# Kernel optimization log

Hardware: AMD Instinct MI355X
Metric: run time of the kernel (lower is better)

Reference implementation:

```python
import jax, jax.numpy as jnp
import numpy as np

B, IN_CH, N, DIM, PH, HID, K = 4, 128, 2048, 256, 64, 1024, 16
EPS = 1e-5


def conv1(x, w, b):
    # 1x1 Conv1d: x (B,C,N), w (O,C) -> (B,O,N)
    return jnp.einsum('oc,bcn->bon', w, x) + b[None, :, None]


def conv2(x, w, b):
    # 1x1 Conv2d: x (B,C,N,K), w (O,C) -> (B,O,N,K)
    return jnp.einsum('oc,bcnk->bonk', w, x) + b[None, :, None, None]


def bn2(x, g, beta, mean, var):
    # eval-mode BatchNorm2d over channel dim of (B,C,N,K)
    scale = g * jax.lax.rsqrt(var + EPS)
    return x * scale[None, :, None, None] + (beta - mean * scale)[None, :, None, None]


def query_knn(pos, k):
    # pos: (B,3,N). Returns (B,N,K) indices of k nearest neighbors (incl. self).
    p = jnp.transpose(pos, (0, 2, 1))                     # (B,N,3)
    sq = jnp.sum(p * p, axis=-1)                          # (B,N)
    dist = sq[:, :, None] + sq[:, None, :] - 2.0 * jnp.einsum('bnc,bmc->bnm', p, p)
    _, idx = jax.lax.top_k(-dist, k)                      # smallest distances first
    return idx


def group(feat, idx):
    # feat: (B,C,N), idx: (B,N,K) -> (B,C,N,K) where out[b,c,i,k]=feat[b,c,idx[b,i,k]]
    b, c, n = feat.shape
    k = idx.shape[-1]
    ib = jnp.broadcast_to(idx.reshape(b, 1, n * k), (b, c, n * k))
    return jnp.take_along_axis(feat, ib, axis=2).reshape(b, c, n, k)


def setup_inputs() -> dict:
    key = jax.random.key(0)
    ks = jax.random.split(key, 12)
    s = 0.02
    return {
        'x': jax.random.normal(ks[0], (B, IN_CH, N), jnp.float32),
        'pos': jax.random.normal(ks[1], (B, 3, N), jnp.float32),
        'ls_w': jax.random.normal(ks[2], (DIM, IN_CH), jnp.float32) * s,
        'ls_b': jnp.zeros((DIM,), jnp.float32),
        'kw': jax.random.normal(ks[3], (DIM, DIM), jnp.float32) * s,
        'kb': jnp.zeros((DIM,), jnp.float32),
        'qw': jax.random.normal(ks[4], (DIM, DIM), jnp.float32) * s,
        'qb': jnp.zeros((DIM,), jnp.float32),
        'vw': jax.random.normal(ks[5], (DIM, DIM), jnp.float32) * s,
        'vb': jnp.zeros((DIM,), jnp.float32),
        'pw1': jax.random.normal(ks[6], (PH, 3), jnp.float32) * s,
        'pb1': jnp.zeros((PH,), jnp.float32),
        'pg': jnp.ones((PH,), jnp.float32),
        'pbeta': jnp.zeros((PH,), jnp.float32),
        'pmean': jnp.zeros((PH,), jnp.float32),
        'pvar': jnp.ones((PH,), jnp.float32),
        'pw2': jax.random.normal(ks[7], (DIM, PH), jnp.float32) * s,
        'pb2': jnp.zeros((DIM,), jnp.float32),
        'aw1': jax.random.normal(ks[8], (HID, DIM), jnp.float32) * s,
        'ab1': jnp.zeros((HID,), jnp.float32),
        'ag': jnp.ones((HID,), jnp.float32),
        'abeta': jnp.zeros((HID,), jnp.float32),
        'amean': jnp.zeros((HID,), jnp.float32),
        'avar': jnp.ones((HID,), jnp.float32),
        'aw2': jax.random.normal(ks[9], (DIM, HID), jnp.float32) * s,
        'ab2': jnp.zeros((DIM,), jnp.float32),
        'lw': jax.random.normal(ks[10], (IN_CH, DIM), jnp.float32) * s,
        'lb': jnp.zeros((IN_CH,), jnp.float32),
    }


def reference(x, pos, ls_w, ls_b, kw, kb, qw, qb, vw, vb,
              pw1, pb1, pg, pbeta, pmean, pvar, pw2, pb2,
              aw1, ab1, ag, abeta, amean, avar, aw2, ab2, lw, lb):
    identity = x
    h = conv1(x, ls_w, ls_b)                              # (B,DIM,N)
    idx = query_knn(pos, K)                               # (B,N,K) int32
    key_f = group(conv1(h, kw, kb), idx)                  # (B,DIM,N,K)
    value = conv1(h, vw, vb)                              # (B,DIM,N)
    query = conv1(h, qw, qb)                              # (B,DIM,N)
    qk_rel = query[:, :, :, None] - key_f                 # (B,DIM,N,K)
    pos_rel = pos[:, :, :, None] - group(pos, idx)        # (B,3,N,K)
    pe = conv2(jax.nn.relu(bn2(conv2(pos_rel, pw1, pb1), pg, pbeta, pmean, pvar)), pw2, pb2)
    attn = conv2(jax.nn.relu(bn2(conv2(qk_rel + pe, aw1, ab1), ag, abeta, amean, avar)), aw2, ab2)
    attn = jax.nn.softmax(attn, axis=-1)                  # softmax over K
    val_g = group(value, idx) + pe                        # (B,DIM,N,K)
    agg = jnp.sum(attn * val_g, axis=-1)                  # (B,DIM,N)
    y = conv1(agg, lw, lb)                                # (B,IN_CH,N)
    return y + identity
```

## Files before the change

### kernel.cpp

```cpp
#include <hip/hip_runtime.h>
#include <hip/hip_bf16.h>
#include <math.h>

#define B_    4
#define CIN   128
#define NPTS  2048
#define DIM   256
#define PH    64
#define HIDN  1024
#define KNN_  16
#define BN    (B_*NPTS)
#define CC    (BN*KNN_)
#define EPS_  1e-5f

typedef __bf16 bf16;
typedef __bf16 bf16x8 __attribute__((ext_vector_type(8)));
typedef __bf16 bf16x4 __attribute__((ext_vector_type(4)));
typedef float  f32x4  __attribute__((ext_vector_type(4)));

__global__ __launch_bounds__(256) void prep_kernel(
    const float* __restrict__ ls_w, const float* __restrict__ kw,
    const float* __restrict__ qw,   const float* __restrict__ vw,
    const float* __restrict__ pw2,  const float* __restrict__ aw1,
    const float* __restrict__ aw2,  const float* __restrict__ lw,
    const float* __restrict__ pb1,  const float* __restrict__ pg,
    const float* __restrict__ pbeta,const float* __restrict__ pmean,
    const float* __restrict__ pvar,
    const float* __restrict__ ab1,  const float* __restrict__ ag,
    const float* __restrict__ abeta,const float* __restrict__ amean,
    const float* __restrict__ avar,
    bf16* ls_wb, bf16* kwb, bf16* qwb, bf16* vwb,
    bf16* pw2b, bf16* aw1b, bf16* aw2b, bf16* lwb,
    float* pe_scale, float* pe_shift, float* at_scale, float* at_shift)
{
  long e = (long)blockIdx.x * 256 + threadIdx.x;
  if (e < 32768)  { ls_wb[e] = (bf16)ls_w[e]; return; } e -= 32768;
  if (e < 65536)  { kwb[e]   = (bf16)kw[e];   return; } e -= 65536;
  if (e < 65536)  { qwb[e]   = (bf16)qw[e];   return; } e -= 65536;
  if (e < 65536)  { vwb[e]   = (bf16)vw[e];   return; } e -= 65536;
  if (e < 16384)  { pw2b[e]  = (bf16)pw2[e];  return; } e -= 16384;
  if (e < 262144) { aw1b[e]  = (bf16)aw1[e];  return; } e -= 262144;
  if (e < 262144) { aw2b[e]  = (bf16)aw2[e];  return; } e -= 262144;
  if (e < 32768)  { lwb[e]   = (bf16)lw[e];   return; } e -= 32768;
  if (e < 64) {
    float sc = pg[e] * rsqrtf(pvar[e] + EPS_);
    pe_scale[e] = sc;
    pe_shift[e] = sc * pb1[e] + pbeta[e] - pmean[e] * sc;
    return;
  } e -= 64;
  if (e < 1024) {
    float sc = ag[e] * rsqrtf(avar[e] + EPS_);
    at_scale[e] = sc;
    at_shift[e] = sc * ab1[e] + abeta[e] - amean[e] * sc;
  }
}

__global__ __launch_bounds__(256) void transpose_x_kernel(
    const float* __restrict__ x, bf16* __restrict__ xT)
{
  long e = (long)blockIdx.x * 256 + threadIdx.x;
  int ch = (int)(e & (CIN - 1));
  long i = e >> 7;
  int n = (int)(i & (NPTS - 1));
  int b = (int)(i >> 11);
  xT[e] = (bf16)x[((long)b * CIN + ch) * NPTS + n];
}

__global__ __launch_bounds__(256) void knn_kernel(
    const float* __restrict__ pos, int* __restrict__ idx_out)
{
  __shared__ float px[NPTS], py[NPTS], pz[NPTS];
  const int tid = threadIdx.x;
  const int lane = tid & 63, wave = tid >> 6;
  const int q = blockIdx.x * 4 + wave;
  const int b = q >> 11;
  const int n = q & (NPTS - 1);
  const float* p = pos + (long)b * 3 * NPTS;
  for (int j = tid; j < NPTS; j += 256) {
    px[j] = p[j]; py[j] = p[NPTS + j]; pz[j] = p[2 * NPTS + j];
  }
  __syncthreads();
  float qx = px[n], qy = py[n], qz = pz[n];
  float qs = qx * qx + qy * qy + qz * qz;
  float d[32];
#pragma unroll
  for (int j = 0; j < 32; ++j) {
    int pt = j * 64 + lane;
    float x = px[pt], y = py[pt], z = pz[pt];
    float s2 = x * x + y * y + z * z;
    float dt = qx * x + qy * y + qz * z;
    d[j] = qs + s2 - 2.f * dt;
  }
  for (int r = 0; r < KNN_; ++r) {
    float bv = 1e30f; int bj = 0;
#pragma unroll
    for (int j = 0; j < 32; ++j)
      if (d[j] < bv) { bv = d[j]; bj = j; }
    int bi = bj * 64 + lane;
#pragma unroll
    for (int off = 32; off >= 1; off >>= 1) {
      float ov = __shfl_xor(bv, off);
      int   oi = __shfl_xor(bi, off);
      if (ov < bv || (ov == bv && oi < bi)) { bv = ov; bi = oi; }
    }
    if (lane == 0) idx_out[(long)q * KNN_ + r] = bi;
#pragma unroll
    for (int j = 0; j < 32; ++j)
      if (bi == j * 64 + lane) d[j] = 1e30f;
  }
}

template<int KD, bool OBF16>
__global__ __launch_bounds__(256) void gemmT_kernel(
    const bf16* __restrict__ inT, const bf16* __restrict__ Wb,
    const float* __restrict__ bias, void* __restrict__ outp, int O)
{
  const int tid = threadIdx.x;
  const int lane = tid & 63, wave = tid >> 6;
  const int row16 = lane & 15, grp = lane >> 4;
  const long i0 = (long)blockIdx.x * 64 + (wave & 1) * 32;
  const long o0 = (long)blockIdx.y * 64 + (wave >> 1) * 32;
  f32x4 acc[2][2] = {};
  const bf16* a0p = inT + (i0 + row16) * KD + grp * 8;
  const bf16* a1p = a0p + 16 * KD;
  const bf16* b0p = Wb + (o0 + row16) * KD + grp * 8;
  const bf16* b1p = b0p + 16 * KD;
#pragma unroll
  for (int ks = 0; ks < KD / 32; ++ks) {
    bf16x8 a0 = *(const bf16x8*)(a0p + ks * 32);
    bf16x8 a1 = *(const bf16x8*)(a1p + ks * 32);
    bf16x8 b0 = *(const bf16x8*)(b0p + ks * 32);
    bf16x8 b1 = *(const bf16x8*)(b1p + ks * 32);
    acc[0][0] = __builtin_amdgcn_mfma_f32_16x16x32_bf16(a0, b0, acc[0][0], 0, 0, 0);
    acc[0][1] = __builtin_amdgcn_mfma_f32_16x16x32_bf16(a0, b1, acc[0][1], 0, 0, 0);
    acc[1][0] = __builtin_amdgcn_mfma_f32_16x16x32_bf16(a1, b0, acc[1][0], 0, 0, 0);
    acc[1][1] = __builtin_amdgcn_mfma_f32_16x16x32_bf16(a1, b1, acc[1][1], 0, 0, 0);
  }
#pragma unroll
  for (int ot = 0; ot < 2; ++ot) {
    long o = o0 + ot * 16 + row16;
    float bv = bias[o];
#pragma unroll
    for (int it = 0; it < 2; ++it) {
#pragma unroll
      for (int r = 0; r < 4; ++r) {
        long i = i0 + it * 16 + grp * 4 + r;
        float v = acc[it][ot][r] + bv;
        if (OBF16) ((bf16*)outp)[i * O + o] = (bf16)v;
        else       ((float*)outp)[i * O + o] = v;
      }
    }
  }
}

__global__ __launch_bounds__(256, 2) void attn_fused_kernel(
    const bf16* __restrict__ qT, const bf16* __restrict__ kT,
    const bf16* __restrict__ vTb, const float* __restrict__ pos,
    const int* __restrict__ idx, const float* __restrict__ pw1,
    const float* __restrict__ pe_scale, const float* __restrict__ pe_shift,
    const bf16* __restrict__ pw2b, const float* __restrict__ pb2,
    const bf16* __restrict__ aw1b, const bf16* __restrict__ aw2b,
    const float* __restrict__ at_scale, const float* __restrict__ at_shift,
    const float* __restrict__ ab2, bf16* __restrict__ aggT)
{
  __shared__ __align__(16) bf16 u_lds[64][264];
  __shared__ __align__(16) bf16 tbuf[64 * 136];
  __shared__ float rel_lds[64][4];
  __shared__ int   idx_lds[64];
  bf16 (*t_lds)[136]  = (bf16(*)[136])tbuf;
  bf16 (*hid_lds)[72] = (bf16(*)[72])tbuf;

  const int tid = threadIdx.x;
  const int lane = tid & 63, wave = tid >> 6;
  const int row16 = lane & 15, grp = lane >> 4;
  const long c0 = (long)blockIdx.x * 64;
  const int bn0 = blockIdx.x * 4;
  const int b = bn0 >> 11;
  const float* pB = pos + (long)b * 3 * NPTS;
  const int os = wave * 64;

  if (tid < 64) {
    int nb = idx[c0 + tid];
    idx_lds[tid] = nb;
    int n = (bn0 + (tid >> 4)) & (NPTS - 1);
    rel_lds[tid][0] = pB[n] - pB[nb];
    rel_lds[tid][1] = pB[NPTS + n] - pB[NPTS + nb];
    rel_lds[tid][2] = pB[2 * NPTS + n] - pB[2 * NPTS + nb];
  }
#pragma unroll
  for (int it = 0; it < 8; ++it) {
    int id = it * 256 + tid;
    int col = id >> 5, ch16 = id & 31;
    int nb = idx[c0 + col];
    *(bf16x8*)&u_lds[col][ch16 * 8] =
        *(const bf16x8*)(kT + ((long)b * NPTS + nb) * DIM + ch16 * 8);
  }
  __syncthreads();

  {
    int c = tid & 63, jq = tid >> 6;
    float rx = rel_lds[c][0], ry = rel_lds[c][1], rz = rel_lds[c][2];
#pragma unroll
    for (int jj = 0; jj < 16; ++jj) {
      int j = jq * 16 + jj;
      float v = pw1[j * 3] * rx + pw1[j * 3 + 1] * ry + pw1[j * 3 + 2] * rz;
      v = pe_scale[j] * v + pe_shift[j];
      hid_lds[c][j] = (bf16)fmaxf(v, 0.f);
    }
  }
  __syncthreads();

  f32x4 accpe[4][4] = {};
#pragma unroll
  for (int ks = 0; ks < 2; ++ks) {
    bf16x8 ah[4];
#pragma unroll
    for (int ct = 0; ct < 4; ++ct)
      ah[ct] = *(const bf16x8*)&hid_lds[ct * 16 + row16][ks * 32 + grp * 8];
#pragma unroll
    for (int ot = 0; ot < 4; ++ot) {
      bf16x8 bw = *(const bf16x8*)(pw2b + (long)(os + ot * 16 + row16) * PH + ks * 32 + grp * 8);
#pragma unroll
      for (int ct = 0; ct < 4; ++ct)
        accpe[ct][ot] = __builtin_amdgcn_mfma_f32_16x16x32_bf16(ah[ct], bw, accpe[ct][ot], 0, 0, 0);
    }
  }

  bf16x4 pe_bf[4][4];
#pragma unroll
  for (int ot = 0; ot < 4; ++ot) {
    int o = os + ot * 16 + row16;
    float pb2v = pb2[o];
#pragma unroll
    for (int ct = 0; ct < 4; ++ct) {
      float qv = (float)qT[(long)(bn0 + ct) * DIM + o];
#pragma unroll
      for (int r = 0; r < 4; ++r) {
        int c = ct * 16 + grp * 4 + r;
        float pev = accpe[ct][ot][r] + pb2v;
        float kv = (float)u_lds[c][o];
        u_lds[c][o] = (bf16)(qv - kv + pev);
        pe_bf[ct][ot][r] = (bf16)pev;
      }
    }
  }
  __syncthreads();

  const int hs = wave * 32;
  f32x4 acc2[4][4] = {};
  for (int jc = 0; jc < 8; ++jc) {
    const int hg = jc * 128 + hs;
    f32x4 acc1[4][2] = {};
#pragma unroll
    for (int ks = 0; ks < 8; ++ks) {
      bf16x8 bu[4], aw[2];
#pragma unroll
      for (int ct = 0; ct < 4; ++ct)
        bu[ct] = *(const bf16x8*)&u_lds[ct * 16 + row16][ks * 32 + grp * 8];
#pragma unroll
      for (int jt = 0; jt < 2; ++jt)
        aw[jt] = *(const bf16x8*)(aw1b + (long)(hg + jt * 16 + row16) * DIM + ks * 32 + grp * 8);
#pragma unroll
      for (int ct = 0; ct < 4; ++ct)
#pragma unroll
        for (int jt = 0; jt < 2; ++jt)
          acc1[ct][jt] = __builtin_amdgcn_mfma_f32_16x16x32_bf16(aw[jt], bu[ct], acc1[ct][jt], 0, 0, 0);
    }
#pragma unroll
    for (int jt = 0; jt < 2; ++jt) {
      f32x4 sc4 = *(const f32x4*)&at_scale[hg + jt * 16 + grp * 4];
      f32x4 sh4 = *(const f32x4*)&at_shift[hg + jt * 16 + grp * 4];
#pragma unroll
      for (int ct = 0; ct < 4; ++ct) {
        bf16x4 pk;
#pragma unroll
        for (int r = 0; r < 4; ++r) {
          float v = sc4[r] * acc1[ct][jt][r] + sh4[r];
          pk[r] = (bf16)fmaxf(v, 0.f);
        }
        *(bf16x4*)&t_lds[ct * 16 + row16][hs + jt * 16 + grp * 4] = pk;
      }
    }
    __syncthreads();
#pragma unroll
    for (int ks2 = 0; ks2 < 4; ++ks2) {
      bf16x8 a2[4], b2;
#pragma unroll
      for (int ct = 0; ct < 4; ++ct)
        a2[ct] = *(const bf16x8*)&t_lds[ct * 16 + row16][ks2 * 32 + grp * 8];
#pragma unroll
      for (int ot = 0; ot < 4; ++ot) {
        b2 = *(const bf16x8*)(aw2b + (long)(os + ot * 16 + row16) * HIDN + jc * 128 + ks2 * 32 + grp * 8);
#pragma unroll
        for (int ct = 0; ct < 4; ++ct)
          acc2[ct][ot] = __builtin_amdgcn_mfma_f32_16x16x32_bf16(a2[ct], b2, acc2[ct][ot], 0, 0, 0);
      }
    }
    __syncthreads();
  }

#pragma unroll
  for (int ct = 0; ct < 4; ++ct) {
#pragma unroll
    for (int ot = 0; ot < 4; ++ot) {
      int o = os + ot * 16 + row16;
      float ab = ab2[o];
      float l[4];
      float m = -1e30f;
#pragma unroll
      for (int r = 0; r < 4; ++r) {
        l[r] = acc2[ct][ot][r] + ab;
        m = fmaxf(m, l[r]);
      }
      m = fmaxf(m, __shfl_xor(m, 16));
      m = fmaxf(m, __shfl_xor(m, 32));
      float s = 0.f;
#pragma unroll
      for (int r = 0; r < 4; ++r) { l[r] = expf(l[r] - m); s += l[r]; }
      s += __shfl_xor(s, 16);
      s += __shfl_xor(s, 32);
      float inv = 1.f / s;
      float agg = 0.f;
#pragma unroll
      for (int r = 0; r < 4; ++r) {
        int c = ct * 16 + grp * 4 + r;
        int nb = idx_lds[c];
        float vv = (float)vTb[((long)b * NPTS + nb) * DIM + o];
        agg += l[r] * (vv + (float)pe_bf[ct][ot][r]);
      }
      agg *= inv;
      agg += __shfl_xor(agg, 16);
      agg += __shfl_xor(agg, 32);
      if (grp == 0) aggT[(long)(bn0 + ct) * DIM + o] = (bf16)agg;
    }
  }
}

__global__ __launch_bounds__(256) void final_kernel(
    const bf16* __restrict__ aggT, const bf16* __restrict__ lwb,
    const float* __restrict__ lb, const float* __restrict__ x,
    float* __restrict__ out)
{
  const int tid = threadIdx.x;
  const int lane = tid & 63, wave = tid >> 6;
  const int row16 = lane & 15, grp = lane >> 4;
  const long i0 = (long)blockIdx.x * 64 + (wave & 1) * 32;
  const int o0 = blockIdx.y * 64 + (wave >> 1) * 32;
  f32x4 acc[2][2] = {};
  const bf16* a0p = aggT + (i0 + row16) * DIM + grp * 8;
  const bf16* a1p = a0p + 16 * DIM;
  const bf16* b0p = lwb + (long)(o0 + row16) * DIM + grp * 8;
  const bf16* b1p = b0p + 16 * DIM;
#pragma unroll
  for (int ks = 0; ks < 8; ++ks) {
    bf16x8 a0 = *(const bf16x8*)(a0p + ks * 32);
    bf16x8 a1 = *(const bf16x8*)(a1p + ks * 32);
    bf16x8 b0 = *(const bf16x8*)(b0p + ks * 32);
    bf16x8 b1 = *(const bf16x8*)(b1p + ks * 32);
    acc[0][0] = __builtin_amdgcn_mfma_f32_16x16x32_bf16(a0, b0, acc[0][0], 0, 0, 0);
    acc[0][1] = __builtin_amdgcn_mfma_f32_16x16x32_bf16(a0, b1, acc[0][1], 0, 0, 0);
    acc[1][0] = __builtin_amdgcn_mfma_f32_16x16x32_bf16(a1, b0, acc[1][0], 0, 0, 0);
    acc[1][1] = __builtin_amdgcn_mfma_f32_16x16x32_bf16(a1, b1, acc[1][1], 0, 0, 0);
  }
#pragma unroll
  for (int ot = 0; ot < 2; ++ot) {
    int o = o0 + ot * 16 + row16;
    float bv = lb[o];
#pragma unroll
    for (int it = 0; it < 2; ++it) {
#pragma unroll
      for (int r = 0; r < 4; ++r) {
        long i = i0 + it * 16 + grp * 4 + r;
        int bb = (int)(i >> 11);
        int n = (int)(i & (NPTS - 1));
        long off = ((long)bb * CIN + o) * NPTS + n;
        out[off] = acc[it][ot][r] + bv + x[off];
      }
    }
  }
}

extern "C" void kernel_launch(void* const* d_in, const int* in_sizes, int n_in,
                              void* d_out, int out_size, void* d_ws, size_t ws_size,
                              hipStream_t stream)
{
  const float* x     = (const float*)d_in[0];
  const float* pos   = (const float*)d_in[1];
  const float* ls_w  = (const float*)d_in[2];
  const float* ls_b  = (const float*)d_in[3];
  const float* kw    = (const float*)d_in[4];
  const float* kb    = (const float*)d_in[5];
  const float* qw    = (const float*)d_in[6];
  const float* qb    = (const float*)d_in[7];
  const float* vw    = (const float*)d_in[8];
  const float* vb    = (const float*)d_in[9];
  const float* pw1   = (const float*)d_in[10];
  const float* pb1   = (const float*)d_in[11];
  const float* pg    = (const float*)d_in[12];
  const float* pbeta = (const float*)d_in[13];
  const float* pmean = (const float*)d_in[14];
  const float* pvar  = (const float*)d_in[15];
  const float* pw2   = (const float*)d_in[16];
  const float* pb2   = (const float*)d_in[17];
  const float* aw1   = (const float*)d_in[18];
  const float* ab1   = (const float*)d_in[19];
  const float* ag    = (const float*)d_in[20];
  const float* abeta = (const float*)d_in[21];
  const float* amean = (const float*)d_in[22];
  const float* avar  = (const float*)d_in[23];
  const float* aw2   = (const float*)d_in[24];
  const float* ab2   = (const float*)d_in[25];
  const float* lw    = (const float*)d_in[26];
  const float* lb    = (const float*)d_in[27];

  char* ws = (char*)d_ws;
  size_t off = 0;
  auto alloc = [&](size_t bytes) -> void* {
    void* p = ws + off;
    off = (off + bytes + 255) & ~(size_t)255;
    return p;
  };

  bf16* ls_wb = (bf16*)alloc(32768 * 2);
  bf16* kwb   = (bf16*)alloc(65536 * 2);
  bf16* qwb   = (bf16*)alloc(65536 * 2);
  bf16* vwb   = (bf16*)alloc(65536 * 2);
  bf16* pw2b  = (bf16*)alloc(16384 * 2);
  bf16* aw1b  = (bf16*)alloc(262144 * 2);
  bf16* aw2b  = (bf16*)alloc(262144 * 2);
  bf16* lwb   = (bf16*)alloc(32768 * 2);
  float* pe_scale = (float*)alloc(64 * 4);
  float* pe_shift = (float*)alloc(64 * 4);
  float* at_scale = (float*)alloc(1024 * 4);
  float* at_shift = (float*)alloc(1024 * 4);
  int*  idx  = (int*)alloc((size_t)CC * 4);
  bf16* xT   = (bf16*)alloc((size_t)BN * CIN * 2);
  bf16* hT   = (bf16*)alloc((size_t)BN * DIM * 2);
  bf16* qT   = (bf16*)alloc((size_t)BN * DIM * 2);
  bf16* kT   = (bf16*)alloc((size_t)BN * DIM * 2);
  bf16* vTb  = (bf16*)alloc((size_t)BN * DIM * 2);
  bf16* aggT = (bf16*)alloc((size_t)BN * DIM * 2);

  prep_kernel<<<dim3((803904 + 255) / 256), 256, 0, stream>>>(
      ls_w, kw, qw, vw, pw2, aw1, aw2, lw,
      pb1, pg, pbeta, pmean, pvar, ab1, ag, abeta, amean, avar,
      ls_wb, kwb, qwb, vwb, pw2b, aw1b, aw2b, lwb,
      pe_scale, pe_shift, at_scale, at_shift);

  transpose_x_kernel<<<dim3(BN * CIN / 256), 256, 0, stream>>>(x, xT);

  knn_kernel<<<dim3(BN / 4), 256, 0, stream>>>(pos, idx);

  gemmT_kernel<128, true><<<dim3(BN / 64, DIM / 64), 256, 0, stream>>>(xT, ls_wb, ls_b, hT, DIM);

  gemmT_kernel<256, true><<<dim3(BN / 64, DIM / 64), 256, 0, stream>>>(hT, qwb, qb, qT, DIM);
  gemmT_kernel<256, true><<<dim3(BN / 64, DIM / 64), 256, 0, stream>>>(hT, kwb, kb, kT, DIM);
  gemmT_kernel<256, true><<<dim3(BN / 64, DIM / 64), 256, 0, stream>>>(hT, vwb, vb, vTb, DIM);

  attn_fused_kernel<<<dim3(CC / 64), 256, 0, stream>>>(
      qT, kT, vTb, pos, idx, pw1, pe_scale, pe_shift, pw2b, pb2,
      aw1b, aw2b, at_scale, at_shift, ab2, aggT);

  final_kernel<<<dim3(BN / 64, CIN / 64), 256, 0, stream>>>(aggT, lwb, lb, x, (float*)d_out);
}
```

Baseline: 513.9 us.

## Precompose attention first layer with q/k/pos projections to shrink per-neighbor GEMM

Uses linearity of aw1 over (q - k + pe): precomputes aw1·Wq and aw1·Wk as weight products, computes per-point A1q and A1k (BN x 1024), and composes aw1·pw2 into a 1024x64 matrix. The per-neighbor first attention GEMM drops from K=256 to K=64 over the hidden features, plus gathered A1k rows. The trade is extra point-level GEMMs and larger gathered rows (1024 bf16 per neighbor) with different bf16 rounding. Occupancy hint raised to 4 blocks since the large u_lds buffer is removed.

```diff
diff --git a/kernel.cpp b/kernel.cpp
--- a/kernel.cpp
+++ b/kernel.cpp
@@ -19,29 +19,36 @@
 typedef float  f32x4  __attribute__((ext_vector_type(4)));
 
 __global__ __launch_bounds__(256) void prep_kernel(
-    const float* __restrict__ ls_w, const float* __restrict__ kw,
-    const float* __restrict__ qw,   const float* __restrict__ vw,
+    const float* __restrict__ ls_w, const float* __restrict__ qw,
+    const float* __restrict__ kw,   const float* __restrict__ vw,
     const float* __restrict__ pw2,  const float* __restrict__ aw1,
     const float* __restrict__ aw2,  const float* __restrict__ lw,
+    const float* __restrict__ qb,   const float* __restrict__ kb,
+    const float* __restrict__ pb2,
     const float* __restrict__ pb1,  const float* __restrict__ pg,
     const float* __restrict__ pbeta,const float* __restrict__ pmean,
     const float* __restrict__ pvar,
     const float* __restrict__ ab1,  const float* __restrict__ ag,
     const float* __restrict__ abeta,const float* __restrict__ amean,
     const float* __restrict__ avar,
-    bf16* ls_wb, bf16* kwb, bf16* qwb, bf16* vwb,
-    bf16* pw2b, bf16* aw1b, bf16* aw2b, bf16* lwb,
-    float* pe_scale, float* pe_shift, float* at_scale, float* at_shift)
+    bf16* ls_wb, bf16* vwb, bf16* qwt, bf16* kwt,
+    bf16* pw2b, bf16* pw2t, bf16* aw1b, bf16* aw2b, bf16* lwb,
+    float* pe_scale, float* pe_shift, float* at_scale, float* at_shift,
+    float* bq, float* bk, float* zeros)
 {
   long e = (long)blockIdx.x * 256 + threadIdx.x;
   if (e < 32768)  { ls_wb[e] = (bf16)ls_w[e]; return; } e -= 32768;
-  if (e < 65536)  { kwb[e]   = (bf16)kw[e];   return; } e -= 65536;
-  if (e < 65536)  { qwb[e]   = (bf16)qw[e];   return; } e -= 65536;
   if (e < 65536)  { vwb[e]   = (bf16)vw[e];   return; } e -= 65536;
-  if (e < 16384)  { pw2b[e]  = (bf16)pw2[e];  return; } e -= 16384;
-  if (e < 262144) { aw1b[e]  = (bf16)aw1[e];  return; } e -= 262144;
-  if (e < 262144) { aw2b[e]  = (bf16)aw2[e];  return; } e -= 262144;
-  if (e < 32768)  { lwb[e]   = (bf16)lw[e];   return; } e -= 32768;
+  if (e < 65536)  { int c = (int)(e >> 8), o = (int)(e & 255);
+                    qwt[e] = (bf16)qw[o * 256 + c]; return; } e -= 65536;
+  if (e < 65536)  { int c = (int)(e >> 8), o = (int)(e & 255);
+                    kwt[e] = (bf16)kw[o * 256 + c]; return; } e -= 65536;
+  if (e < 16384)  { pw2b[e] = (bf16)pw2[e];   return; } e -= 16384;
+  if (e < 16384)  { int ph = (int)(e >> 8), o = (int)(e & 255);
+                    pw2t[e] = (bf16)pw2[o * 64 + ph]; return; } e -= 16384;
+  if (e < 262144) { aw1b[e] = (bf16)aw1[e];   return; } e -= 262144;
+  if (e < 262144) { aw2b[e] = (bf16)aw2[e];   return; } e -= 262144;
+  if (e < 32768)  { lwb[e]  = (bf16)lw[e];    return; } e -= 32768;
   if (e < 64) {
     float sc = pg[e] * rsqrtf(pvar[e] + EPS_);
     pe_scale[e] = sc;
@@ -52,7 +59,19 @@
     float sc = ag[e] * rsqrtf(avar[e] + EPS_);
     at_scale[e] = sc;
     at_shift[e] = sc * ab1[e] + abeta[e] - amean[e] * sc;
-  }
+    return;
+  } e -= 1024;
+  if (e < 1024) {
+    float s = 0.f;
+    for (int o = 0; o < 256; ++o) s += aw1[e * 256 + o] * (qb[o] + pb2[o]);
+    bq[e] = s; return;
+  } e -= 1024;
+  if (e < 1024) {
+    float s = 0.f;
+    for (int o = 0; o < 256; ++o) s += aw1[e * 256 + o] * kb[o];
+    bk[e] = s; return;
+  } e -= 1024;
+  if (e < 1024) { zeros[e] = 0.f; }
 }
 
 __global__ __launch_bounds__(256) void transpose_x_kernel(
@@ -153,22 +172,20 @@
   }
 }
 
-__global__ __launch_bounds__(256, 2) void attn_fused_kernel(
-    const bf16* __restrict__ qT, const bf16* __restrict__ kT,
+__global__ __launch_bounds__(256, 4) void attn_fused_kernel(
     const bf16* __restrict__ vTb, const float* __restrict__ pos,
     const int* __restrict__ idx, const float* __restrict__ pw1,
     const float* __restrict__ pe_scale, const float* __restrict__ pe_shift,
     const bf16* __restrict__ pw2b, const float* __restrict__ pb2,
-    const bf16* __restrict__ aw1b, const bf16* __restrict__ aw2b,
+    const bf16* __restrict__ Mwb, const bf16* __restrict__ A1q,
+    const bf16* __restrict__ A1k, const bf16* __restrict__ aw2b,
     const float* __restrict__ at_scale, const float* __restrict__ at_shift,
     const float* __restrict__ ab2, bf16* __restrict__ aggT)
 {
-  __shared__ __align__(16) bf16 u_lds[64][264];
-  __shared__ __align__(16) bf16 tbuf[64 * 136];
+  __shared__ __align__(16) bf16 hid_lds[64][72];
+  __shared__ __align__(16) bf16 t_lds[64][136];
   __shared__ float rel_lds[64][4];
   __shared__ int   idx_lds[64];
-  bf16 (*t_lds)[136]  = (bf16(*)[136])tbuf;
-  bf16 (*hid_lds)[72] = (bf16(*)[72])tbuf;
 
   const int tid = threadIdx.x;
   const int lane = tid & 63, wave = tid >> 6;
@@ -178,6 +195,7 @@
   const int b = bn0 >> 11;
   const float* pB = pos + (long)b * 3 * NPTS;
   const int os = wave * 64;
+  const int hs = wave * 32;
 
   if (tid < 64) {
     int nb = idx[c0 + tid];
@@ -187,14 +205,6 @@
     rel_lds[tid][1] = pB[NPTS + n] - pB[NPTS + nb];
     rel_lds[tid][2] = pB[2 * NPTS + n] - pB[2 * NPTS + nb];
   }
-#pragma unroll
-  for (int it = 0; it < 8; ++it) {
-    int id = it * 256 + tid;
-    int col = id >> 5, ch16 = id & 31;
-    int nb = idx[c0 + col];
-    *(bf16x8*)&u_lds[col][ch16 * 8] =
-        *(const bf16x8*)(kT + ((long)b * NPTS + nb) * DIM + ch16 * 8);
-  }
   __syncthreads();
 
   {
@@ -210,6 +220,10 @@
   }
   __syncthreads();
 
+  int nbv[4];
+#pragma unroll
+  for (int ct = 0; ct < 4; ++ct) nbv[ct] = idx_lds[ct * 16 + row16];
+
   f32x4 accpe[4][4] = {};
 #pragma unroll
   for (int ks = 0; ks < 2; ++ks) {
@@ -225,57 +239,49 @@
         accpe[ct][ot] = __builtin_amdgcn_mfma_f32_16x16x32_bf16(ah[ct], bw, accpe[ct][ot], 0, 0, 0);
     }
   }
-
   bf16x4 pe_bf[4][4];
 #pragma unroll
   for (int ot = 0; ot < 4; ++ot) {
-    int o = os + ot * 16 + row16;
-    float pb2v = pb2[o];
-#pragma unroll
-    for (int ct = 0; ct < 4; ++ct) {
-      float qv = (float)qT[(long)(bn0 + ct) * DIM + o];
-#pragma unroll
-      for (int r = 0; r < 4; ++r) {
-        int c = ct * 16 + grp * 4 + r;
-        float pev = accpe[ct][ot][r] + pb2v;
-        float kv = (float)u_lds[c][o];
-        u_lds[c][o] = (bf16)(qv - kv + pev);
-        pe_bf[ct][ot][r] = (bf16)pev;
-      }
-    }
-  }
-  __syncthreads();
-
-  const int hs = wave * 32;
+    float pb2v = pb2[os + ot * 16 + row16];
+#pragma unroll
+    for (int ct = 0; ct < 4; ++ct)
+#pragma unroll
+      for (int r = 0; r < 4; ++r)
+        pe_bf[ct][ot][r] = (bf16)(accpe[ct][ot][r] + pb2v);
+  }
+
   f32x4 acc2[4][4] = {};
   for (int jc = 0; jc < 8; ++jc) {
     const int hg = jc * 128 + hs;
     f32x4 acc1[4][2] = {};
 #pragma unroll
-    for (int ks = 0; ks < 8; ++ks) {
-      bf16x8 bu[4], aw[2];
+    for (int ks = 0; ks < 2; ++ks) {
+      bf16x8 mw[2], hf[4];
+#pragma unroll
+      for (int jt = 0; jt < 2; ++jt)
+        mw[jt] = *(const bf16x8*)(Mwb + (long)(hg + jt * 16 + row16) * PH + ks * 32 + grp * 8);
 #pragma unroll
       for (int ct = 0; ct < 4; ++ct)
-        bu[ct] = *(const bf16x8*)&u_lds[ct * 16 + row16][ks * 32 + grp * 8];
-#pragma unroll
-      for (int jt = 0; jt < 2; ++jt)
-        aw[jt] = *(const bf16x8*)(aw1b + (long)(hg + jt * 16 + row16) * DIM + ks * 32 + grp * 8);
+        hf[ct] = *(const bf16x8*)&hid_lds[ct * 16 + row16][ks * 32 + grp * 8];
 #pragma unroll
       for (int ct = 0; ct < 4; ++ct)
 #pragma unroll
         for (int jt = 0; jt < 2; ++jt)
-          acc1[ct][jt] = __builtin_amdgcn_mfma_f32_16x16x32_bf16(aw[jt], bu[ct], acc1[ct][jt], 0, 0, 0);
+          acc1[ct][jt] = __builtin_amdgcn_mfma_f32_16x16x32_bf16(mw[jt], hf[ct], acc1[ct][jt], 0, 0, 0);
     }
 #pragma unroll
     for (int jt = 0; jt < 2; ++jt) {
-      f32x4 sc4 = *(const f32x4*)&at_scale[hg + jt * 16 + grp * 4];
-      f32x4 sh4 = *(const f32x4*)&at_shift[hg + jt * 16 + grp * 4];
+      int jb = hg + jt * 16 + grp * 4;
+      f32x4 sc4 = *(const f32x4*)&at_scale[jb];
+      f32x4 sh4 = *(const f32x4*)&at_shift[jb];
 #pragma unroll
       for (int ct = 0; ct < 4; ++ct) {
+        bf16x4 aq = *(const bf16x4*)(A1q + (long)(bn0 + ct) * HIDN + jb);
+        bf16x4 ak = *(const bf16x4*)(A1k + ((long)b * NPTS + nbv[ct]) * HIDN + jb);
         bf16x4 pk;
 #pragma unroll
         for (int r = 0; r < 4; ++r) {
-          float v = sc4[r] * acc1[ct][jt][r] + sh4[r];
+          float v = sc4[r] * (acc1[ct][jt][r] + (float)aq[r] - (float)ak[r]) + sh4[r];
           pk[r] = (bf16)fmaxf(v, 0.f);
         }
         *(bf16x4*)&t_lds[ct * 16 + row16][hs + jt * 16 + grp * 4] = pk;
@@ -422,10 +428,11 @@
   };
 
   bf16* ls_wb = (bf16*)alloc(32768 * 2);
-  bf16* kwb   = (bf16*)alloc(65536 * 2);
-  bf16* qwb   = (bf16*)alloc(65536 * 2);
   bf16* vwb   = (bf16*)alloc(65536 * 2);
+  bf16* qwt   = (bf16*)alloc(65536 * 2);
+  bf16* kwt   = (bf16*)alloc(65536 * 2);
   bf16* pw2b  = (bf16*)alloc(16384 * 2);
+  bf16* pw2t  = (bf16*)alloc(16384 * 2);
   bf16* aw1b  = (bf16*)alloc(262144 * 2);
   bf16* aw2b  = (bf16*)alloc(262144 * 2);
   bf16* lwb   = (bf16*)alloc(32768 * 2);
@@ -433,19 +440,25 @@
   float* pe_shift = (float*)alloc(64 * 4);
   float* at_scale = (float*)alloc(1024 * 4);
   float* at_shift = (float*)alloc(1024 * 4);
+  float* bq    = (float*)alloc(1024 * 4);
+  float* bk    = (float*)alloc(1024 * 4);
+  float* zeros = (float*)alloc(1024 * 4);
   int*  idx  = (int*)alloc((size_t)CC * 4);
   bf16* xT   = (bf16*)alloc((size_t)BN * CIN * 2);
   bf16* hT   = (bf16*)alloc((size_t)BN * DIM * 2);
-  bf16* qT   = (bf16*)alloc((size_t)BN * DIM * 2);
-  bf16* kT   = (bf16*)alloc((size_t)BN * DIM * 2);
   bf16* vTb  = (bf16*)alloc((size_t)BN * DIM * 2);
+  bf16* Waq  = (bf16*)alloc((size_t)HIDN * DIM * 2);
+  bf16* Wak  = (bf16*)alloc((size_t)HIDN * DIM * 2);
+  bf16* Mwb  = (bf16*)alloc((size_t)HIDN * PH * 2);
+  bf16* A1q  = (bf16*)alloc((size_t)BN * HIDN * 2);
+  bf16* A1k  = (bf16*)alloc((size_t)BN * HIDN * 2);
   bf16* aggT = (bf16*)alloc((size_t)BN * DIM * 2);
 
-  prep_kernel<<<dim3((803904 + 255) / 256), 256, 0, stream>>>(
-      ls_w, kw, qw, vw, pw2, aw1, aw2, lw,
+  prep_kernel<<<dim3((823360 + 255) / 256), 256, 0, stream>>>(
+      ls_w, qw, kw, vw, pw2, aw1, aw2, lw, qb, kb, pb2,
       pb1, pg, pbeta, pmean, pvar, ab1, ag, abeta, amean, avar,
-      ls_wb, kwb, qwb, vwb, pw2b, aw1b, aw2b, lwb,
-      pe_scale, pe_shift, at_scale, at_shift);
+      ls_wb, vwb, qwt, kwt, pw2b, pw2t, aw1b, aw2b, lwb,
+      pe_scale, pe_shift, at_scale, at_shift, bq, bk, zeros);
 
   transpose_x_kernel<<<dim3(BN * CIN / 256), 256, 0, stream>>>(x, xT);
 
@@ -453,13 +466,17 @@
 
   gemmT_kernel<128, true><<<dim3(BN / 64, DIM / 64), 256, 0, stream>>>(xT, ls_wb, ls_b, hT, DIM);
 
-  gemmT_kernel<256, true><<<dim3(BN / 64, DIM / 64), 256, 0, stream>>>(hT, qwb, qb, qT, DIM);
-  gemmT_kernel<256, true><<<dim3(BN / 64, DIM / 64), 256, 0, stream>>>(hT, kwb, kb, kT, DIM);
+  gemmT_kernel<256, true><<<dim3(HIDN / 64, DIM / 64), 256, 0, stream>>>(aw1b, qwt, zeros, Waq, DIM);
+  gemmT_kernel<256, true><<<dim3(HIDN / 64, DIM / 64), 256, 0, stream>>>(aw1b, kwt, zeros, Wak, DIM);
+  gemmT_kernel<256, true><<<dim3(HIDN / 64, PH / 64), 256, 0, stream>>>(aw1b, pw2t, zeros, Mwb, PH);
+
   gemmT_kernel<256, true><<<dim3(BN / 64, DIM / 64), 256, 0, stream>>>(hT, vwb, vb, vTb, DIM);
+  gemmT_kernel<256, true><<<dim3(BN / 64, HIDN / 64), 256, 0, stream>>>(hT, Waq, bq, A1q, HIDN);
+  gemmT_kernel<256, true><<<dim3(BN / 64, HIDN / 64), 256, 0, stream>>>(hT, Wak, bk, A1k, HIDN);
 
   attn_fused_kernel<<<dim3(CC / 64), 256, 0, stream>>>(
-      qT, kT, vTb, pos, idx, pw1, pe_scale, pe_shift, pw2b, pb2,
-      aw1b, aw2b, at_scale, at_shift, ab2, aggT);
+      vTb, pos, idx, pw1, pe_scale, pe_shift, pw2b, pb2,
+      Mwb, A1q, A1k, aw2b, at_scale, at_shift, ab2, aggT);
 
   final_kernel<<<dim3(BN / 64, CIN / 64), 256, 0, stream>>>(aggT, lwb, lb, x, (float*)d_out);
 }
```

New measurement: 656.8 us. +27.8%, slower.

## Fuse Q/K/V projections into one GEMM and gather keys directly in attention

Applied to the files above, without the earlier changes.

The three separate Q, K and V projection GEMMs become a single GEMM over a concatenated 768-row weight, writing an interleaved qkvT buffer. The attention kernel no longer stages gathered key rows in LDS before building the attention input. It computes a second, transposed copy of the positional-encoding MFMA result so each lane can read q and k rows directly and write u_lds with vector stores. Launch bounds rise to 3 blocks per CU, which cuts launches and an LDS pass at the cost of extra MFMAs and register pressure.

```diff
diff --git a/kernel.cpp b/kernel.cpp
--- a/kernel.cpp
+++ b/kernel.cpp
@@ -11,6 +11,7 @@
 #define KNN_  16
 #define BN    (B_*NPTS)
 #define CC    (BN*KNN_)
+#define QKV   768
 #define EPS_  1e-5f
 
 typedef __bf16 bf16;
@@ -19,29 +20,35 @@
 typedef float  f32x4  __attribute__((ext_vector_type(4)));
 
 __global__ __launch_bounds__(256) void prep_kernel(
-    const float* __restrict__ ls_w, const float* __restrict__ kw,
-    const float* __restrict__ qw,   const float* __restrict__ vw,
+    const float* __restrict__ ls_w, const float* __restrict__ qw,
+    const float* __restrict__ kw,   const float* __restrict__ vw,
     const float* __restrict__ pw2,  const float* __restrict__ aw1,
     const float* __restrict__ aw2,  const float* __restrict__ lw,
+    const float* __restrict__ qb,   const float* __restrict__ kb,
+    const float* __restrict__ vb,
     const float* __restrict__ pb1,  const float* __restrict__ pg,
     const float* __restrict__ pbeta,const float* __restrict__ pmean,
     const float* __restrict__ pvar,
     const float* __restrict__ ab1,  const float* __restrict__ ag,
     const float* __restrict__ abeta,const float* __restrict__ amean,
     const float* __restrict__ avar,
-    bf16* ls_wb, bf16* kwb, bf16* qwb, bf16* vwb,
-    bf16* pw2b, bf16* aw1b, bf16* aw2b, bf16* lwb,
-    float* pe_scale, float* pe_shift, float* at_scale, float* at_shift)
+    bf16* ls_wb, bf16* wqkvb, bf16* pw2b, bf16* aw1b, bf16* aw2b, bf16* lwb,
+    float* pe_scale, float* pe_shift, float* at_scale, float* at_shift,
+    float* bqkv)
 {
   long e = (long)blockIdx.x * 256 + threadIdx.x;
   if (e < 32768)  { ls_wb[e] = (bf16)ls_w[e]; return; } e -= 32768;
-  if (e < 65536)  { kwb[e]   = (bf16)kw[e];   return; } e -= 65536;
-  if (e < 65536)  { qwb[e]   = (bf16)qw[e];   return; } e -= 65536;
-  if (e < 65536)  { vwb[e]   = (bf16)vw[e];   return; } e -= 65536;
-  if (e < 16384)  { pw2b[e]  = (bf16)pw2[e];  return; } e -= 16384;
-  if (e < 262144) { aw1b[e]  = (bf16)aw1[e];  return; } e -= 262144;
-  if (e < 262144) { aw2b[e]  = (bf16)aw2[e];  return; } e -= 262144;
-  if (e < 32768)  { lwb[e]   = (bf16)lw[e];   return; } e -= 32768;
+  if (e < 196608) {
+    int row = (int)(e >> 8), col = (int)(e & 255);
+    float v = (row < 256) ? qw[row * 256 + col]
+            : (row < 512) ? kw[(row - 256) * 256 + col]
+                          : vw[(row - 512) * 256 + col];
+    wqkvb[e] = (bf16)v; return;
+  } e -= 196608;
+  if (e < 16384)  { pw2b[e] = (bf16)pw2[e];  return; } e -= 16384;
+  if (e < 262144) { aw1b[e] = (bf16)aw1[e];  return; } e -= 262144;
+  if (e < 262144) { aw2b[e] = (bf16)aw2[e];  return; } e -= 262144;
+  if (e < 32768)  { lwb[e]  = (bf16)lw[e];   return; } e -= 32768;
   if (e < 64) {
     float sc = pg[e] * rsqrtf(pvar[e] + EPS_);
     pe_scale[e] = sc;
@@ -52,6 +59,10 @@
     float sc = ag[e] * rsqrtf(avar[e] + EPS_);
     at_scale[e] = sc;
     at_shift[e] = sc * ab1[e] + abeta[e] - amean[e] * sc;
+    return;
+  } e -= 1024;
+  if (e < 768) {
+    bqkv[e] = (e < 256) ? qb[e] : (e < 512) ? kb[e - 256] : vb[e - 512];
   }
 }
 
@@ -153,9 +164,8 @@
   }
 }
 
-__global__ __launch_bounds__(256, 2) void attn_fused_kernel(
-    const bf16* __restrict__ qT, const bf16* __restrict__ kT,
-    const bf16* __restrict__ vTb, const float* __restrict__ pos,
+__global__ __launch_bounds__(256, 3) void attn_fused_kernel(
+    const bf16* __restrict__ qkvT, const float* __restrict__ pos,
     const int* __restrict__ idx, const float* __restrict__ pw1,
     const float* __restrict__ pe_scale, const float* __restrict__ pe_shift,
     const bf16* __restrict__ pw2b, const float* __restrict__ pb2,
@@ -178,6 +188,7 @@
   const int b = bn0 >> 11;
   const float* pB = pos + (long)b * 3 * NPTS;
   const int os = wave * 64;
+  const int hs = wave * 32;
 
   if (tid < 64) {
     int nb = idx[c0 + tid];
@@ -187,14 +198,6 @@
     rel_lds[tid][1] = pB[NPTS + n] - pB[NPTS + nb];
     rel_lds[tid][2] = pB[2 * NPTS + n] - pB[2 * NPTS + nb];
   }
-#pragma unroll
-  for (int it = 0; it < 8; ++it) {
-    int id = it * 256 + tid;
-    int col = id >> 5, ch16 = id & 31;
-    int nb = idx[c0 + col];
-    *(bf16x8*)&u_lds[col][ch16 * 8] =
-        *(const bf16x8*)(kT + ((long)b * NPTS + nb) * DIM + ch16 * 8);
-  }
   __syncthreads();
 
   {
@@ -211,42 +214,56 @@
   __syncthreads();
 
   f32x4 accpe[4][4] = {};
+  f32x4 accpeT[4][4] = {};
 #pragma unroll
   for (int ks = 0; ks < 2; ++ks) {
-    bf16x8 ah[4];
+    bf16x8 ah[4], bw[4];
 #pragma unroll
     for (int ct = 0; ct < 4; ++ct)
       ah[ct] = *(const bf16x8*)&hid_lds[ct * 16 + row16][ks * 32 + grp * 8];
 #pragma unroll
+    for (int ot = 0; ot < 4; ++ot)
+      bw[ot] = *(const bf16x8*)(pw2b + (long)(os + ot * 16 + row16) * PH + ks * 32 + grp * 8);
+#pragma unroll
+    for (int ct = 0; ct < 4; ++ct)
+#pragma unroll
+      for (int ot = 0; ot < 4; ++ot) {
+        accpe[ct][ot]  = __builtin_amdgcn_mfma_f32_16x16x32_bf16(ah[ct], bw[ot], accpe[ct][ot], 0, 0, 0);
+        accpeT[ct][ot] = __builtin_amdgcn_mfma_f32_16x16x32_bf16(bw[ot], ah[ct], accpeT[ct][ot], 0, 0, 0);
+      }
+  }
+
+  bf16x4 pe_bf[4][4];
+#pragma unroll
+  for (int ot = 0; ot < 4; ++ot) {
+    float pb2v = pb2[os + ot * 16 + row16];
+#pragma unroll
+    for (int ct = 0; ct < 4; ++ct)
+#pragma unroll
+      for (int r = 0; r < 4; ++r)
+        pe_bf[ct][ot][r] = (bf16)(accpe[ct][ot][r] + pb2v);
+  }
+
+#pragma unroll
+  for (int ct = 0; ct < 4; ++ct) {
+    int nb = idx_lds[ct * 16 + row16];
+    const bf16* krow = qkvT + ((long)b * NPTS + nb) * QKV + 256 + os;
+    const bf16* qrow = qkvT + (long)(bn0 + ct) * QKV + os;
+#pragma unroll
     for (int ot = 0; ot < 4; ++ot) {
-      bf16x8 bw = *(const bf16x8*)(pw2b + (long)(os + ot * 16 + row16) * PH + ks * 32 + grp * 8);
-#pragma unroll
-      for (int ct = 0; ct < 4; ++ct)
-        accpe[ct][ot] = __builtin_amdgcn_mfma_f32_16x16x32_bf16(ah[ct], bw, accpe[ct][ot], 0, 0, 0);
-    }
-  }
-
-  bf16x4 pe_bf[4][4];
-#pragma unroll
-  for (int ot = 0; ot < 4; ++ot) {
-    int o = os + ot * 16 + row16;
-    float pb2v = pb2[o];
-#pragma unroll
-    for (int ct = 0; ct < 4; ++ct) {
-      float qv = (float)qT[(long)(bn0 + ct) * DIM + o];
-#pragma unroll
-      for (int r = 0; r < 4; ++r) {
-        int c = ct * 16 + grp * 4 + r;
-        float pev = accpe[ct][ot][r] + pb2v;
-        float kv = (float)u_lds[c][o];
-        u_lds[c][o] = (bf16)(qv - kv + pev);
-        pe_bf[ct][ot][r] = (bf16)pev;
-      }
+      int o4 = ot * 16 + grp * 4;
+      bf16x4 k4 = *(const bf16x4*)(krow + o4);
+      bf16x4 q4 = *(const bf16x4*)(qrow + o4);
+      f32x4 pb4 = *(const f32x4*)&pb2[os + o4];
+      bf16x4 u4;
+#pragma unroll
+      for (int r = 0; r < 4; ++r)
+        u4[r] = (bf16)((float)q4[r] - (float)k4[r] + accpeT[ct][ot][r] + pb4[r]);
+      *(bf16x4*)&u_lds[ct * 16 + row16][os + o4] = u4;
     }
   }
   __syncthreads();
 
-  const int hs = wave * 32;
   f32x4 acc2[4][4] = {};
   for (int jc = 0; jc < 8; ++jc) {
     const int hg = jc * 128 + hs;
@@ -268,8 +285,9 @@
     }
 #pragma unroll
     for (int jt = 0; jt < 2; ++jt) {
-      f32x4 sc4 = *(const f32x4*)&at_scale[hg + jt * 16 + grp * 4];
-      f32x4 sh4 = *(const f32x4*)&at_shift[hg + jt * 16 + grp * 4];
+      int jb = hg + jt * 16 + grp * 4;
+      f32x4 sc4 = *(const f32x4*)&at_scale[jb];
+      f32x4 sh4 = *(const f32x4*)&at_shift[jb];
 #pragma unroll
       for (int ct = 0; ct < 4; ++ct) {
         bf16x4 pk;
@@ -325,7 +343,7 @@
       for (int r = 0; r < 4; ++r) {
         int c = ct * 16 + grp * 4 + r;
         int nb = idx_lds[c];
-        float vv = (float)vTb[((long)b * NPTS + nb) * DIM + o];
+        float vv = (float)qkvT[((long)b * NPTS + nb) * QKV + 512 + o];
         agg += l[r] * (vv + (float)pe_bf[ct][ot][r]);
       }
       agg *= inv;
@@ -422,9 +440,7 @@
   };
 
   bf16* ls_wb = (bf16*)alloc(32768 * 2);
-  bf16* kwb   = (bf16*)alloc(65536 * 2);
-  bf16* qwb   = (bf16*)alloc(65536 * 2);
-  bf16* vwb   = (bf16*)alloc(65536 * 2);
+  bf16* wqkvb = (bf16*)alloc(196608 * 2);
   bf16* pw2b  = (bf16*)alloc(16384 * 2);
   bf16* aw1b  = (bf16*)alloc(262144 * 2);
   bf16* aw2b  = (bf16*)alloc(262144 * 2);
@@ -433,19 +449,18 @@
   float* pe_shift = (float*)alloc(64 * 4);
   float* at_scale = (float*)alloc(1024 * 4);
   float* at_shift = (float*)alloc(1024 * 4);
+  float* bqkv = (float*)alloc(768 * 4);
   int*  idx  = (int*)alloc((size_t)CC * 4);
   bf16* xT   = (bf16*)alloc((size_t)BN * CIN * 2);
   bf16* hT   = (bf16*)alloc((size_t)BN * DIM * 2);
-  bf16* qT   = (bf16*)alloc((size_t)BN * DIM * 2);
-  bf16* kT   = (bf16*)alloc((size_t)BN * DIM * 2);
-  bf16* vTb  = (bf16*)alloc((size_t)BN * DIM * 2);
+  bf16* qkvT = (bf16*)alloc((size_t)BN * QKV * 2);
   bf16* aggT = (bf16*)alloc((size_t)BN * DIM * 2);
 
-  prep_kernel<<<dim3((803904 + 255) / 256), 256, 0, stream>>>(
-      ls_w, kw, qw, vw, pw2, aw1, aw2, lw,
+  prep_kernel<<<dim3((804672 + 255) / 256), 256, 0, stream>>>(
+      ls_w, qw, kw, vw, pw2, aw1, aw2, lw, qb, kb, vb,
       pb1, pg, pbeta, pmean, pvar, ab1, ag, abeta, amean, avar,
-      ls_wb, kwb, qwb, vwb, pw2b, aw1b, aw2b, lwb,
-      pe_scale, pe_shift, at_scale, at_shift);
+      ls_wb, wqkvb, pw2b, aw1b, aw2b, lwb,
+      pe_scale, pe_shift, at_scale, at_shift, bqkv);
 
   transpose_x_kernel<<<dim3(BN * CIN / 256), 256, 0, stream>>>(x, xT);
 
@@ -453,12 +468,10 @@
 
   gemmT_kernel<128, true><<<dim3(BN / 64, DIM / 64), 256, 0, stream>>>(xT, ls_wb, ls_b, hT, DIM);
 
-  gemmT_kernel<256, true><<<dim3(BN / 64, DIM / 64), 256, 0, stream>>>(hT, qwb, qb, qT, DIM);
-  gemmT_kernel<256, true><<<dim3(BN / 64, DIM / 64), 256, 0, stream>>>(hT, kwb, kb, kT, DIM);
-  gemmT_kernel<256, true><<<dim3(BN / 64, DIM / 64), 256, 0, stream>>>(hT, vwb, vb, vTb, DIM);
+  gemmT_kernel<256, true><<<dim3(BN / 64, QKV / 64), 256, 0, stream>>>(hT, wqkvb, bqkv, qkvT, QKV);
 
   attn_fused_kernel<<<dim3(CC / 64), 256, 0, stream>>>(
-      qT, kT, vTb, pos, idx, pw1, pe_scale, pe_shift, pw2b, pb2,
+      qkvT, pos, idx, pw1, pe_scale, pe_shift, pw2b, pb2,
       aw1b, aw2b, at_scale, at_shift, ab2, aggT);
 
   final_kernel<<<dim3(BN / 64, CIN / 64), 256, 0, stream>>>(aggT, lwb, lb, x, (float*)d_out);
```

Result: slower. 533.7 us (+3.8%).
